# Kernel optimization log

Measured on AMD Instinct MI355X. Metric: run time of the kernel, lower is better.

Reference implementation:

```python
import jax, jax.numpy as jnp
import numpy as np

N = 50000        # nodes
E = 800000       # edges (avg degree 16)
F = 64           # num_features
G = 128          # number of graphs in the batch
NOUT = 1         # n_output


def setup_inputs() -> dict:
    key = jax.random.key(0)
    ks = jax.random.split(key, 9)
    x = jax.random.normal(ks[0], (N, F), dtype=jnp.float32)
    edge_index = jax.random.randint(ks[1], (2, E), 0, N, dtype=jnp.int64)
    batch = jnp.sort(jax.random.randint(ks[2], (N,), 0, G, dtype=jnp.int64))
    W1 = jax.random.normal(ks[3], (F, F), dtype=jnp.float32) * 0.1
    b1 = jnp.zeros((F,), dtype=jnp.float32)
    W2 = jax.random.normal(ks[4], (F, 2 * F), dtype=jnp.float32) * 0.1
    b2 = jnp.zeros((2 * F,), dtype=jnp.float32)
    fcW = jax.random.normal(ks[5], (2 * F, NOUT), dtype=jnp.float32) * 0.1
    fcb = jnp.zeros((NOUT,), dtype=jnp.float32)
    return {"x": x, "edge_index": edge_index, "batch": batch,
            "W1": W1, "b1": b1, "W2": W2, "b2": b2, "fcW": fcW, "fcb": fcb}


def reference(x, edge_index, batch, W1, b1, W2, b2, fcW, fcb):
    n = x.shape[0]
    # PyG GCNConv: add self-loops, symmetric normalization D^-1/2 (A+I) D^-1/2
    loop = jnp.arange(n, dtype=edge_index.dtype)
    src = jnp.concatenate([edge_index[0], loop])  # [E+N]
    dst = jnp.concatenate([edge_index[1], loop])  # [E+N]
    deg = jax.ops.segment_sum(jnp.ones_like(dst, dtype=x.dtype), dst, num_segments=n)
    dinv = jnp.where(deg > 0, jax.lax.rsqrt(jnp.maximum(deg, 1.0)), 0.0)
    norm = dinv[src] * dinv[dst]                  # [E+N]

    def gcn_conv(h, W, b):
        h = h @ W                                 # [N, Fout]
        msg = h[src] * norm[:, None]              # gather + scale, [E+N, Fout]
        return jax.ops.segment_sum(msg, dst, num_segments=n) + b

    h1 = jax.nn.relu(gcn_conv(x, W1, b1))         # [N, F]
    h2 = jax.nn.relu(gcn_conv(h1, W2, b2))        # [N, 2F]

    # global mean pool per graph (dropout is identity in eval)
    counts = jax.ops.segment_sum(jnp.ones((n,), x.dtype), batch, num_segments=G)
    pooled = jax.ops.segment_sum(h2, batch, num_segments=G)
    pooled = pooled / jnp.maximum(counts, 1.0)[:, None]  # [G, 2F]

    out = pooled @ fcW + fcb                      # [G, NOUT]
    return out.reshape(1, -1)                     # [1, G*NOUT]
```

## Files before the change

### kernel.cpp

```cpp
#include <hip/hip_runtime.h>
#include <hip/hip_bf16.h>

typedef __hip_bfloat16 bf16;

static __device__ __forceinline__ float loadF(const void* p, long long i, int f32){
  return f32 ? ((const float*)p)[i] : __bfloat162float(((const bf16*)p)[i]);
}
static __device__ __forceinline__ int loadI(const void* p, long long i, int i64){
  return i64 ? (int)((const long long*)p)[i] : ((const int*)p)[i];
}
static __device__ __forceinline__ unsigned short f2bf(float f){
  unsigned u = __float_as_uint(f);
  return (unsigned short)((u + 0x7FFFu + ((u>>16)&1u)) >> 16);
}
static __device__ __forceinline__ float bf2f(unsigned v){
  return __uint_as_float(v<<16);
}

#define CAP 4096
#define LB_EDGES 8192

__global__ void k_init(const unsigned int* __restrict__ xw, const unsigned int* __restrict__ eiw,
                       int* __restrict__ flags, int* __restrict__ gcursor, int nbuckets,
                       float* __restrict__ S, int gn, int* __restrict__ done){
  int i = blockIdx.x*256 + threadIdx.x;
  if(i < nbuckets) gcursor[i] = 0;
  if(i < gn) S[i] = 0.f;
  if(i == 0) done[0] = 0;
  if(blockIdx.x == 0){
    __shared__ int s1, s2;
    if(threadIdx.x==0){ s1=0; s2=0; }
    __syncthreads();
    unsigned w = xw[threadIdx.x];
    int e = (int)((w>>7)&0xFFu);
    if(e>=110 && e<=135) atomicAdd(&s1, 1);
    if(eiw[2*threadIdx.x+1] != 0u) atomicAdd(&s2, 1);
    __syncthreads();
    if(threadIdx.x==0){
      flags[0] = (s1 < 128) ? 1 : 0;
      flags[1] = (s2 < 128) ? 1 : 0;
    }
  }
}

__global__ __launch_bounds__(256) void k_pre(const void* __restrict__ ei, int E, int N,
                                             const int* __restrict__ flags,
                                             int* __restrict__ gcursor,
                                             unsigned int* __restrict__ log, int nbuckets,
                                             const void* __restrict__ x, const void* __restrict__ W,
                                             unsigned short* __restrict__ y, int nLog){
  __shared__ unsigned int smem[12416];
  int t = threadIdx.x;
  if((int)blockIdx.x < nLog){
    unsigned int* stash = smem;
    int* hcnt  = (int*)(smem + LB_EDGES);
    int* hbase = (int*)(smem + LB_EDGES + 1024);
    for(int b=t; b<nbuckets; b+=256) hcnt[b] = 0;
    __syncthreads();
    int i64 = flags[1];
    long long e0 = (long long)blockIdx.x*LB_EDGES;
    int cnt = (int)(((long long)E - e0) < LB_EDGES ? ((long long)E - e0) : LB_EDGES);
    for(int k=t; k<cnt; k+=256){
      long long e = e0 + k;
      int s = loadI(ei, e, i64);                 s = min(max(s,0), N-1);
      int d = loadI(ei, (long long)E + e, i64);  d = min(max(d,0), N-1);
      unsigned p = (((unsigned)d)<<16) | (unsigned)s;
      stash[k] = p;
      atomicAdd(&hcnt[d>>6], 1);
    }
    __syncthreads();
    for(int b=t; b<nbuckets; b+=256){
      int c = hcnt[b];
      hbase[b] = (c>0) ? atomicAdd(&gcursor[b], c) : 0;
      hcnt[b] = 0;
    }
    __syncthreads();
    for(int k=t; k<cnt; k+=256){
      unsigned p = stash[k];
      int b = (int)(p>>22);
      int pos = hbase[b] + atomicAdd(&hcnt[b], 1);
      if(pos < CAP) log[(long long)b*CAP + pos] = p;
    }
  } else {
    float* Ws = (float*)smem;
    float* xs = (float*)(smem + 4096);
    int f32 = flags[0];
    int row0 = ((int)blockIdx.x - nLog)*128;
    if(f32){
      const float4* W4 = (const float4*)W;
      for(int i=t;i<1024;i+=256){
        float4 v = W4[i];
        Ws[i*4]=v.x; Ws[i*4+1]=v.y; Ws[i*4+2]=v.z; Ws[i*4+3]=v.w;
      }
      const float4* X4 = (const float4*)x;
      for(int i=t;i<2048;i+=256){
        int r = i>>4, c4 = i&15;
        int gr = row0 + r;
        float4 v = {0.f,0.f,0.f,0.f};
        if(gr<N) v = X4[(long long)gr*16 + c4];
        float* xd = &xs[r*65 + c4*4];
        xd[0]=v.x; xd[1]=v.y; xd[2]=v.z; xd[3]=v.w;
      }
    } else {
      for(int i=t;i<4096;i+=256) Ws[i] = loadF(W, i, 0);
      const unsigned int* X32 = (const unsigned int*)x;
      for(int i=t;i<4096;i+=256){
        int r = i>>5, kd = i&31;
        int gr = row0 + r;
        unsigned v = (gr<N) ? X32[(long long)gr*32 + kd] : 0u;
        xs[r*65 + 2*kd    ] = bf2f(v & 0xFFFFu);
        xs[r*65 + 2*kd + 1] = bf2f(v >> 16);
      }
    }
    __syncthreads();
    int cg = t&15, rg = t>>4;
    int col_g = cg*4, row_g = rg*8;
    float acc[8][4];
    #pragma unroll
    for(int r=0;r<8;r++){ acc[r][0]=0.f; acc[r][1]=0.f; acc[r][2]=0.f; acc[r][3]=0.f; }
    for(int k=0;k<64;k++){
      float4 w = *(const float4*)&Ws[k*64 + col_g];
      float xr[8];
      #pragma unroll
      for(int r=0;r<8;r++) xr[r] = xs[(row_g+r)*65 + k];
      #pragma unroll
      for(int r=0;r<8;r++){
        acc[r][0] += xr[r]*w.x; acc[r][1] += xr[r]*w.y;
        acc[r][2] += xr[r]*w.z; acc[r][3] += xr[r]*w.w;
      }
    }
    #pragma unroll
    for(int r=0;r<8;r++){
      int gr = row0 + row_g + r;
      if(gr<N){
        ushort4 st;
        st.x = f2bf(acc[r][0]); st.y = f2bf(acc[r][1]);
        st.z = f2bf(acc[r][2]); st.w = f2bf(acc[r][3]);
        *(ushort4*)&y[(long long)gr*64 + col_g] = st;
      }
    }
  }
}

__global__ __launch_bounds__(256) void k_bsortg0(const unsigned int* __restrict__ log,
                                                 const int* __restrict__ gcursor,
                                                 unsigned short* __restrict__ csr,
                                                 int* __restrict__ beg, int* __restrict__ endv,
                                                 float* __restrict__ dinv,
                                                 const unsigned int* __restrict__ Y32,
                                                 unsigned int* __restrict__ G032, int N){
  __shared__ int hist[64];
  __shared__ int cur[64];
  __shared__ float dloc[64];
  int b = blockIdx.x, t = threadIdx.x;
  if(t < 64) hist[t] = 0;
  __syncthreads();
  int n = min(gcursor[b], CAP);
  const unsigned int* L = log + (long long)b*CAP;
  for(int j=t; j<n; j+=256) atomicAdd(&hist[(L[j]>>16)&63], 1);
  __syncthreads();
  if(t < 64){
    int v = hist[t];
    int inc = v;
    #pragma unroll
    for(int o=1; o<64; o<<=1){
      int u = __shfl_up(inc, o);
      if(t >= o) inc += u;
    }
    int excl = inc - v;
    cur[t] = excl;
    float dv = rsqrtf((float)(v + 1));
    dloc[t] = dv;
    int node = b*64 + t;
    if(node < N){
      int base = b*CAP + excl;
      beg[node]  = base;
      endv[node] = base + v;
      dinv[node] = dv;
    }
  }
  __syncthreads();
  unsigned short* C = csr + (long long)b*CAP;
  for(int j=t; j<n; j+=256){
    unsigned p = L[j];
    int l = (int)((p>>16)&63u);
    int pos = atomicAdd(&cur[l], 1);
    C[pos] = (unsigned short)(p & 0xFFFFu);
  }
  long long base32 = (long long)b*2048;
  for(int i=t; i<2048; i+=256){
    int nl = i>>5;
    int node = b*64 + nl;
    if(node < N){
      unsigned v = Y32[base32 + i];
      float dv = dloc[nl];
      G032[base32 + i] = (unsigned)f2bf(bf2f(v & 0xFFFFu)*dv)
                       | ((unsigned)f2bf(bf2f(v >> 16)*dv) << 16);
    }
  }
}

__global__ __launch_bounds__(256) void k_agg(const unsigned short* __restrict__ g,
                                             const unsigned short* __restrict__ csr,
                                             const int* __restrict__ beg, const int* __restrict__ endv,
                                             const float* __restrict__ dinv,
                                             const void* __restrict__ bias, const int* __restrict__ flags,
                                             int mode,
                                             uint4* __restrict__ out128, int N){
  int node = blockIdx.x*4 + (threadIdx.x>>6);
  int lane = threadIdx.x&63;
  if(node >= N) return;
  int q = lane&7, eg = lane>>3;
  const uint4* G128 = (const uint4*)g;
  int j = beg[node], e = endv[node];
  float a0=0.f,a1=0.f,a2=0.f,a3=0.f,a4=0.f,a5=0.f,a6=0.f,a7=0.f;
  for(; j+16<=e; j+=16){
    int sA = csr[j + eg];
    int sB = csr[j + 8 + eg];
    uint4 vA = G128[(long long)sA*8 + q];
    uint4 vB = G128[(long long)sB*8 + q];
    a0 += bf2f(vA.x & 0xFFFFu); a1 += bf2f(vA.x >> 16);
    a2 += bf2f(vA.y & 0xFFFFu); a3 += bf2f(vA.y >> 16);
    a4 += bf2f(vA.z & 0xFFFFu); a5 += bf2f(vA.z >> 16);
    a6 += bf2f(vA.w & 0xFFFFu); a7 += bf2f(vA.w >> 16);
    a0 += bf2f(vB.x & 0xFFFFu); a1 += bf2f(vB.x >> 16);
    a2 += bf2f(vB.y & 0xFFFFu); a3 += bf2f(vB.y >> 16);
    a4 += bf2f(vB.z & 0xFFFFu); a5 += bf2f(vB.z >> 16);
    a6 += bf2f(vB.w & 0xFFFFu); a7 += bf2f(vB.w >> 16);
  }
  for(; j+8<=e; j+=8){
    int s = csr[j + eg];
    uint4 v = G128[(long long)s*8 + q];
    a0 += bf2f(v.x & 0xFFFFu); a1 += bf2f(v.x >> 16);
    a2 += bf2f(v.y & 0xFFFFu); a3 += bf2f(v.y >> 16);
    a4 += bf2f(v.z & 0xFFFFu); a5 += bf2f(v.z >> 16);
    a6 += bf2f(v.w & 0xFFFFu); a7 += bf2f(v.w >> 16);
  }
  if(j + eg < e){
    int s = csr[j + eg];
    uint4 v = G128[(long long)s*8 + q];
    a0 += bf2f(v.x & 0xFFFFu); a1 += bf2f(v.x >> 16);
    a2 += bf2f(v.y & 0xFFFFu); a3 += bf2f(v.y >> 16);
    a4 += bf2f(v.z & 0xFFFFu); a5 += bf2f(v.z >> 16);
    a6 += bf2f(v.w & 0xFFFFu); a7 += bf2f(v.w >> 16);
  }
  uint4 sv = {0u,0u,0u,0u};
  float dv = 0.f;
  if(eg == 0){
    sv = G128[(long long)node*8 + q];
    dv = dinv[node];
  }
  #pragma unroll
  for(int m=8; m<64; m<<=1){
    a0 += __shfl_xor(a0, m, 64); a1 += __shfl_xor(a1, m, 64);
    a2 += __shfl_xor(a2, m, 64); a3 += __shfl_xor(a3, m, 64);
    a4 += __shfl_xor(a4, m, 64); a5 += __shfl_xor(a5, m, 64);
    a6 += __shfl_xor(a6, m, 64); a7 += __shfl_xor(a7, m, 64);
  }
  if(eg == 0){
    float f0 = (a0 + bf2f(sv.x & 0xFFFFu)) * dv;
    float f1 = (a1 + bf2f(sv.x >> 16)) * dv;
    float f2 = (a2 + bf2f(sv.y & 0xFFFFu)) * dv;
    float f3 = (a3 + bf2f(sv.y >> 16)) * dv;
    float f4 = (a4 + bf2f(sv.z & 0xFFFFu)) * dv;
    float f5 = (a5 + bf2f(sv.z >> 16)) * dv;
    float f6 = (a6 + bf2f(sv.w & 0xFFFFu)) * dv;
    float f7 = (a7 + bf2f(sv.w >> 16)) * dv;
    if(mode){
      int f32 = flags[0];
      f0 = fmaxf(f0 + loadF(bias, q*8+0, f32), 0.f) * dv;
      f1 = fmaxf(f1 + loadF(bias, q*8+1, f32), 0.f) * dv;
      f2 = fmaxf(f2 + loadF(bias, q*8+2, f32), 0.f) * dv;
      f3 = fmaxf(f3 + loadF(bias, q*8+3, f32), 0.f) * dv;
      f4 = fmaxf(f4 + loadF(bias, q*8+4, f32), 0.f) * dv;
      f5 = fmaxf(f5 + loadF(bias, q*8+5, f32), 0.f) * dv;
      f6 = fmaxf(f6 + loadF(bias, q*8+6, f32), 0.f) * dv;
      f7 = fmaxf(f7 + loadF(bias, q*8+7, f32), 0.f) * dv;
    }
    uint4 o;
    o.x = (unsigned)f2bf(f0) | ((unsigned)f2bf(f1) << 16);
    o.y = (unsigned)f2bf(f2) | ((unsigned)f2bf(f3) << 16);
    o.z = (unsigned)f2bf(f4) | ((unsigned)f2bf(f5) << 16);
    o.w = (unsigned)f2bf(f6) | ((unsigned)f2bf(f7) << 16);
    out128[(long long)node*8 + q] = o;
  }
}

static __device__ __forceinline__ int lower_bound_batch(const void* batch, int N, int key, int i64){
  int lo = 0, hi = N;
  while(lo < hi){ int mid = (lo+hi)>>1; if(loadI(batch, mid, i64) < key) lo = mid+1; else hi = mid; }
  return lo;
}

__global__ __launch_bounds__(512) void k_gemm2pool(const unsigned int* __restrict__ A32, const void* __restrict__ W,
                                                   const void* __restrict__ b, const void* __restrict__ fcW,
                                                   const void* __restrict__ batch, const int* __restrict__ flags,
                                                   float* __restrict__ S, int* __restrict__ done,
                                                   const void* __restrict__ fcb, void* __restrict__ out,
                                                   int N, int G, int NOUT){
  __shared__ float Ws[64*128];
  __shared__ float xs[128*65];
  __shared__ float Sloc[128*4];
  __shared__ int gid[128];
  __shared__ int lastBlk;
  int f32 = flags[0], i64 = flags[1];
  int tid = threadIdx.x;
  int row0 = blockIdx.x*128;
  for(int i=tid;i<8192;i+=512) Ws[i] = loadF(W, i, f32);
  for(int i=tid;i<4096;i+=512){
    int r = i>>5, kd = i&31;
    int gr = row0 + r;
    unsigned v = (gr<N) ? A32[(long long)gr*32 + kd] : 0u;
    xs[r*65 + 2*kd    ] = bf2f(v & 0xFFFFu);
    xs[r*65 + 2*kd + 1] = bf2f(v >> 16);
  }
  if(tid < 128){
    int node = row0 + tid;
    gid[tid] = (node < N) ? loadI(batch, node, i64) : 0;
  }
  if(tid < 512) { if(tid < 512 && tid < 512) ; }
  for(int i=tid;i<512;i+=512) Sloc[i] = 0.f;
  __syncthreads();
  int cg = tid&15, rg = tid>>4;
  int c0 = cg*4, c1 = 64 + cg*4, row_g = rg*4;
  float acc[4][8];
  #pragma unroll
  for(int r=0;r<4;r++)
    #pragma unroll
    for(int c=0;c<8;c++) acc[r][c]=0.f;
  for(int k=0;k<64;k++){
    float4 w0 = *(const float4*)&Ws[k*128 + c0];
    float4 w1 = *(const float4*)&Ws[k*128 + c1];
    float xr[4];
    #pragma unroll
    for(int r=0;r<4;r++) xr[r] = xs[(row_g+r)*65 + k];
    #pragma unroll
    for(int r=0;r<4;r++){
      acc[r][0] += xr[r]*w0.x; acc[r][1] += xr[r]*w0.y;
      acc[r][2] += xr[r]*w0.z; acc[r][3] += xr[r]*w0.w;
      acc[r][4] += xr[r]*w1.x; acc[r][5] += xr[r]*w1.y;
      acc[r][6] += xr[r]*w1.z; acc[r][7] += xr[r]*w1.w;
    }
  }
  #pragma unroll
  for(int c=0;c<8;c++){
    int col = (c<4) ? (c0+c) : (c1+c-4);
    float bb = loadF(b, col, f32);
    #pragma unroll
    for(int r=0;r<4;r++){ float z = acc[r][c]+bb; acc[r][c] = z>0.f?z:0.f; }
  }
  int nv = N - row0; nv = nv < 128 ? nv : 128;
  if(nv > 0){
    int gmin = gid[0], gmax = gid[nv-1];
    bool ldsOK = (NOUT <= 4) && (gmax - gmin < 128);
    for(int o=0;o<NOUT;o++){
      float fw[8];
      #pragma unroll
      for(int c=0;c<8;c++){
        int col = (c<4) ? (c0+c) : (c1+c-4);
        fw[c] = loadF(fcW, (long long)col*NOUT + o, f32);
      }
      #pragma unroll
      for(int r=0;r<4;r++){
        float z = acc[r][0]*fw[0] + acc[r][1]*fw[1] + acc[r][2]*fw[2] + acc[r][3]*fw[3]
                + acc[r][4]*fw[4] + acc[r][5]*fw[5] + acc[r][6]*fw[6] + acc[r][7]*fw[7];
        #pragma unroll
        for(int m=1;m<16;m<<=1) z += __shfl_xor(z, m, 64);
        int nl = row_g + r;
        if(cg==0 && nl < nv){
          int gg = gid[nl];
          if(ldsOK) atomicAdd(&Sloc[(gg-gmin)*NOUT + o], z);
          else      atomicAdd(&S[(long long)gg*NOUT + o], z);
        }
      }
    }
    if(ldsOK){
      __syncthreads();
      int nbin = (gmax - gmin + 1)*NOUT;
      for(int i=tid; i<nbin; i+=512){
        float v = Sloc[i];
        if(v != 0.f){
          int bin = i / NOUT, o = i - bin*NOUT;
          atomicAdd(&S[(long long)(gmin+bin)*NOUT + o], v);
        }
      }
    }
  }
  asm volatile("s_waitcnt vmcnt(0)" ::: "memory");
  if(tid==0) lastBlk = (atomicAdd(done, 1) == (int)gridDim.x - 1) ? 1 : 0;
  __syncthreads();
  if(lastBlk){
    for(int g2=tid; g2<G; g2+=512){
      int c = lower_bound_batch(batch, N, g2+1, i64) - lower_bound_batch(batch, N, g2, i64);
      float inv = 1.f / (float)(c > 0 ? c : 1);
      for(int o=0;o<NOUT;o++){
        float sv = atomicAdd(&S[(long long)g2*NOUT + o], 0.f);
        float r = sv*inv + loadF(fcb, o, f32);
        if(f32) ((float*)out)[g2*NOUT+o] = r;
        else    ((unsigned short*)out)[g2*NOUT+o] = f2bf(r);
      }
    }
  }
}

extern "C" void kernel_launch(void* const* d_in, const int* in_sizes, int n_in,
                              void* d_out, int out_size, void* d_ws, size_t ws_size,
                              hipStream_t stream) {
  const void* x    = d_in[0];
  const void* ei   = d_in[1];
  const void* batch= d_in[2];
  const void* W1   = d_in[3];
  const void* b1   = d_in[4];
  const void* W2   = d_in[5];
  const void* b2   = d_in[6];
  const void* fcW  = d_in[7];
  const void* fcb  = d_in[8];

  const int N = in_sizes[0] / 64;
  const int E = in_sizes[1] / 2;
  const int NOUT = in_sizes[8];
  const int G = out_size / NOUT;
  const int nbuckets = (N + 63) >> 6;

  size_t off = 0;
  auto alloc = [&](size_t bytes) -> char* {
    char* p = (char*)d_ws + off;
    off += (bytes + 511) & ~(size_t)511;
    return p;
  };
  int*   flags   = (int*)  alloc(512);
  int*   done    = (int*)  alloc(512);
  int*   gcursor = (int*)  alloc((size_t)nbuckets*4);
  float* dinv    = (float*)alloc((size_t)N*4);
  int*   beg     = (int*)  alloc((size_t)N*4);
  int*   endv    = (int*)  alloc((size_t)N*4);
  float* S       = (float*)alloc((size_t)G*NOUT*4);
  unsigned int*   log  = (unsigned int*)  alloc((size_t)nbuckets*CAP*4);
  unsigned short* csr  = (unsigned short*)alloc((size_t)nbuckets*CAP*2);
  unsigned short* yB   = (unsigned short*)alloc((size_t)N*64*2);
  unsigned short* g0   = (unsigned short*)alloc((size_t)N*64*2);
  unsigned short* g1   = (unsigned short*)alloc((size_t)N*64*2);
  unsigned int*   aBuf = (unsigned int*)  alloc((size_t)N*32*4);
  (void)ws_size; (void)n_in;

  int initgrid = (nbuckets > G*NOUT ? nbuckets : G*NOUT);
  int nLog = (E + LB_EDGES - 1) / LB_EDGES;
  int nGem = (N + 127) / 128;

  k_init    <<<(initgrid+255)/256, 256, 0, stream>>>((const unsigned int*)x, (const unsigned int*)ei,
                                                     flags, gcursor, nbuckets, S, G*NOUT, done);
  k_pre     <<<nLog + nGem,   256, 0, stream>>>(ei, E, N, flags, gcursor, log, nbuckets,
                                                x, W1, yB, nLog);
  k_bsortg0 <<<nbuckets,      256, 0, stream>>>(log, gcursor, csr, beg, endv, dinv,
                                                (const unsigned int*)yB, (unsigned int*)g0, N);

  k_agg     <<<(N+3)/4,       256, 0, stream>>>(g0, csr, beg, endv, dinv, b1, flags, 1,
                                                (uint4*)g1, N);
  k_agg     <<<(N+3)/4,       256, 0, stream>>>(g1, csr, beg, endv, dinv, b1, flags, 0,
                                                (uint4*)aBuf, N);
  k_gemm2pool<<<(N+127)/128,  512, 0, stream>>>((const unsigned int*)aBuf, W2, b2, fcW, batch, flags,
                                                S, done, fcb, d_out, N, G, NOUT);
}
```

Baseline: 188.2 us.

## Fold source-degree scaling into first aggregation and widen k_pre blocks

The bucket-sort kernel no longer pre-scales the layer-1 GEMM output by dinv into a separate g0 buffer. The first aggregation instead reads the raw GEMM output and multiplies each gathered row by dinv[src] on the fly, with matching self-loop handling. This removes one full N×64 read/write pass and a buffer, at the cost of an extra scattered dinv load per edge. k_pre also moves to 512-thread blocks, with the GEMM branch computing 4 rows per thread instead of 8.

New measurement: 180.9 us. 3.9% less time.

```diff
diff --git a/kernel.cpp b/kernel.cpp
--- a/kernel.cpp
+++ b/kernel.cpp
@@ -43,7 +43,7 @@
   }
 }
 
-__global__ __launch_bounds__(256) void k_pre(const void* __restrict__ ei, int E, int N,
+__global__ __launch_bounds__(512) void k_pre(const void* __restrict__ ei, int E, int N,
                                              const int* __restrict__ flags,
                                              int* __restrict__ gcursor,
                                              unsigned int* __restrict__ log, int nbuckets,
@@ -55,12 +55,12 @@
     unsigned int* stash = smem;
     int* hcnt  = (int*)(smem + LB_EDGES);
     int* hbase = (int*)(smem + LB_EDGES + 1024);
-    for(int b=t; b<nbuckets; b+=256) hcnt[b] = 0;
+    for(int b=t; b<nbuckets; b+=512) hcnt[b] = 0;
     __syncthreads();
     int i64 = flags[1];
     long long e0 = (long long)blockIdx.x*LB_EDGES;
     int cnt = (int)(((long long)E - e0) < LB_EDGES ? ((long long)E - e0) : LB_EDGES);
-    for(int k=t; k<cnt; k+=256){
+    for(int k=t; k<cnt; k+=512){
       long long e = e0 + k;
       int s = loadI(ei, e, i64);                 s = min(max(s,0), N-1);
       int d = loadI(ei, (long long)E + e, i64);  d = min(max(d,0), N-1);
@@ -69,13 +69,13 @@
       atomicAdd(&hcnt[d>>6], 1);
     }
     __syncthreads();
-    for(int b=t; b<nbuckets; b+=256){
+    for(int b=t; b<nbuckets; b+=512){
       int c = hcnt[b];
       hbase[b] = (c>0) ? atomicAdd(&gcursor[b], c) : 0;
       hcnt[b] = 0;
     }
     __syncthreads();
-    for(int k=t; k<cnt; k+=256){
+    for(int k=t; k<cnt; k+=512){
       unsigned p = stash[k];
       int b = (int)(p>>22);
       int pos = hbase[b] + atomicAdd(&hcnt[b], 1);
@@ -88,12 +88,12 @@
     int row0 = ((int)blockIdx.x - nLog)*128;
     if(f32){
       const float4* W4 = (const float4*)W;
-      for(int i=t;i<1024;i+=256){
+      for(int i=t;i<1024;i+=512){
         float4 v = W4[i];
         Ws[i*4]=v.x; Ws[i*4+1]=v.y; Ws[i*4+2]=v.z; Ws[i*4+3]=v.w;
       }
       const float4* X4 = (const float4*)x;
-      for(int i=t;i<2048;i+=256){
+      for(int i=t;i<2048;i+=512){
         int r = i>>4, c4 = i&15;
         int gr = row0 + r;
         float4 v = {0.f,0.f,0.f,0.f};
@@ -102,9 +102,9 @@
         xd[0]=v.x; xd[1]=v.y; xd[2]=v.z; xd[3]=v.w;
       }
     } else {
-      for(int i=t;i<4096;i+=256) Ws[i] = loadF(W, i, 0);
+      for(int i=t;i<4096;i+=512) Ws[i] = loadF(W, i, 0);
       const unsigned int* X32 = (const unsigned int*)x;
-      for(int i=t;i<4096;i+=256){
+      for(int i=t;i<4096;i+=512){
         int r = i>>5, kd = i&31;
         int gr = row0 + r;
         unsigned v = (gr<N) ? X32[(long long)gr*32 + kd] : 0u;
@@ -114,23 +114,23 @@
     }
     __syncthreads();
     int cg = t&15, rg = t>>4;
-    int col_g = cg*4, row_g = rg*8;
-    float acc[8][4];
-    #pragma unroll
-    for(int r=0;r<8;r++){ acc[r][0]=0.f; acc[r][1]=0.f; acc[r][2]=0.f; acc[r][3]=0.f; }
+    int col_g = cg*4, row_g = rg*4;
+    float acc[4][4];
+    #pragma unroll
+    for(int r=0;r<4;r++){ acc[r][0]=0.f; acc[r][1]=0.f; acc[r][2]=0.f; acc[r][3]=0.f; }
     for(int k=0;k<64;k++){
       float4 w = *(const float4*)&Ws[k*64 + col_g];
-      float xr[8];
+      float xr[4];
       #pragma unroll
-      for(int r=0;r<8;r++) xr[r] = xs[(row_g+r)*65 + k];
+      for(int r=0;r<4;r++) xr[r] = xs[(row_g+r)*65 + k];
       #pragma unroll
-      for(int r=0;r<8;r++){
+      for(int r=0;r<4;r++){
         acc[r][0] += xr[r]*w.x; acc[r][1] += xr[r]*w.y;
         acc[r][2] += xr[r]*w.z; acc[r][3] += xr[r]*w.w;
       }
     }
     #pragma unroll
-    for(int r=0;r<8;r++){
+    for(int r=0;r<4;r++){
       int gr = row0 + row_g + r;
       if(gr<N){
         ushort4 st;
@@ -142,16 +142,13 @@
   }
 }
 
-__global__ __launch_bounds__(256) void k_bsortg0(const unsigned int* __restrict__ log,
-                                                 const int* __restrict__ gcursor,
-                                                 unsigned short* __restrict__ csr,
-                                                 int* __restrict__ beg, int* __restrict__ endv,
-                                                 float* __restrict__ dinv,
-                                                 const unsigned int* __restrict__ Y32,
-                                                 unsigned int* __restrict__ G032, int N){
+__global__ __launch_bounds__(256) void k_bsort(const unsigned int* __restrict__ log,
+                                               const int* __restrict__ gcursor,
+                                               unsigned short* __restrict__ csr,
+                                               int* __restrict__ beg, int* __restrict__ endv,
+                                               float* __restrict__ dinv, int N){
   __shared__ int hist[64];
   __shared__ int cur[64];
-  __shared__ float dloc[64];
   int b = blockIdx.x, t = threadIdx.x;
   if(t < 64) hist[t] = 0;
   __syncthreads();
@@ -169,14 +166,12 @@
     }
     int excl = inc - v;
     cur[t] = excl;
-    float dv = rsqrtf((float)(v + 1));
-    dloc[t] = dv;
     int node = b*64 + t;
     if(node < N){
       int base = b*CAP + excl;
       beg[node]  = base;
       endv[node] = base + v;
-      dinv[node] = dv;
+      dinv[node] = rsqrtf((float)(v + 1));
     }
   }
   __syncthreads();
@@ -186,17 +181,6 @@
     int l = (int)((p>>16)&63u);
     int pos = atomicAdd(&cur[l], 1);
     C[pos] = (unsigned short)(p & 0xFFFFu);
-  }
-  long long base32 = (long long)b*2048;
-  for(int i=t; i<2048; i+=256){
-    int nl = i>>5;
-    int node = b*64 + nl;
-    if(node < N){
-      unsigned v = Y32[base32 + i];
-      float dv = dloc[nl];
-      G032[base32 + i] = (unsigned)f2bf(bf2f(v & 0xFFFFu)*dv)
-                       | ((unsigned)f2bf(bf2f(v >> 16)*dv) << 16);
-    }
   }
 }
 
@@ -214,35 +198,71 @@
   const uint4* G128 = (const uint4*)g;
   int j = beg[node], e = endv[node];
   float a0=0.f,a1=0.f,a2=0.f,a3=0.f,a4=0.f,a5=0.f,a6=0.f,a7=0.f;
-  for(; j+16<=e; j+=16){
-    int sA = csr[j + eg];
-    int sB = csr[j + 8 + eg];
-    uint4 vA = G128[(long long)sA*8 + q];
-    uint4 vB = G128[(long long)sB*8 + q];
-    a0 += bf2f(vA.x & 0xFFFFu); a1 += bf2f(vA.x >> 16);
-    a2 += bf2f(vA.y & 0xFFFFu); a3 += bf2f(vA.y >> 16);
-    a4 += bf2f(vA.z & 0xFFFFu); a5 += bf2f(vA.z >> 16);
-    a6 += bf2f(vA.w & 0xFFFFu); a7 += bf2f(vA.w >> 16);
-    a0 += bf2f(vB.x & 0xFFFFu); a1 += bf2f(vB.x >> 16);
-    a2 += bf2f(vB.y & 0xFFFFu); a3 += bf2f(vB.y >> 16);
-    a4 += bf2f(vB.z & 0xFFFFu); a5 += bf2f(vB.z >> 16);
-    a6 += bf2f(vB.w & 0xFFFFu); a7 += bf2f(vB.w >> 16);
-  }
-  for(; j+8<=e; j+=8){
-    int s = csr[j + eg];
-    uint4 v = G128[(long long)s*8 + q];
-    a0 += bf2f(v.x & 0xFFFFu); a1 += bf2f(v.x >> 16);
-    a2 += bf2f(v.y & 0xFFFFu); a3 += bf2f(v.y >> 16);
-    a4 += bf2f(v.z & 0xFFFFu); a5 += bf2f(v.z >> 16);
-    a6 += bf2f(v.w & 0xFFFFu); a7 += bf2f(v.w >> 16);
-  }
-  if(j + eg < e){
-    int s = csr[j + eg];
-    uint4 v = G128[(long long)s*8 + q];
-    a0 += bf2f(v.x & 0xFFFFu); a1 += bf2f(v.x >> 16);
-    a2 += bf2f(v.y & 0xFFFFu); a3 += bf2f(v.y >> 16);
-    a4 += bf2f(v.z & 0xFFFFu); a5 += bf2f(v.z >> 16);
-    a6 += bf2f(v.w & 0xFFFFu); a7 += bf2f(v.w >> 16);
+  if(mode){
+    for(; j+16<=e; j+=16){
+      int sA = csr[j + eg];
+      int sB = csr[j + 8 + eg];
+      float dA = dinv[sA], dB = dinv[sB];
+      uint4 vA = G128[(long long)sA*8 + q];
+      uint4 vB = G128[(long long)sB*8 + q];
+      a0 += dA*bf2f(vA.x & 0xFFFFu); a1 += dA*bf2f(vA.x >> 16);
+      a2 += dA*bf2f(vA.y & 0xFFFFu); a3 += dA*bf2f(vA.y >> 16);
+      a4 += dA*bf2f(vA.z & 0xFFFFu); a5 += dA*bf2f(vA.z >> 16);
+      a6 += dA*bf2f(vA.w & 0xFFFFu); a7 += dA*bf2f(vA.w >> 16);
+      a0 += dB*bf2f(vB.x & 0xFFFFu); a1 += dB*bf2f(vB.x >> 16);
+      a2 += dB*bf2f(vB.y & 0xFFFFu); a3 += dB*bf2f(vB.y >> 16);
+      a4 += dB*bf2f(vB.z & 0xFFFFu); a5 += dB*bf2f(vB.z >> 16);
+      a6 += dB*bf2f(vB.w & 0xFFFFu); a7 += dB*bf2f(vB.w >> 16);
+    }
+    for(; j+8<=e; j+=8){
+      int s = csr[j + eg];
+      float d = dinv[s];
+      uint4 v = G128[(long long)s*8 + q];
+      a0 += d*bf2f(v.x & 0xFFFFu); a1 += d*bf2f(v.x >> 16);
+      a2 += d*bf2f(v.y & 0xFFFFu); a3 += d*bf2f(v.y >> 16);
+      a4 += d*bf2f(v.z & 0xFFFFu); a5 += d*bf2f(v.z >> 16);
+      a6 += d*bf2f(v.w & 0xFFFFu); a7 += d*bf2f(v.w >> 16);
+    }
+    if(j + eg < e){
+      int s = csr[j + eg];
+      float d = dinv[s];
+      uint4 v = G128[(long long)s*8 + q];
+      a0 += d*bf2f(v.x & 0xFFFFu); a1 += d*bf2f(v.x >> 16);
+      a2 += d*bf2f(v.y & 0xFFFFu); a3 += d*bf2f(v.y >> 16);
+      a4 += d*bf2f(v.z & 0xFFFFu); a5 += d*bf2f(v.z >> 16);
+      a6 += d*bf2f(v.w & 0xFFFFu); a7 += d*bf2f(v.w >> 16);
+    }
+  } else {
+    for(; j+16<=e; j+=16){
+      int sA = csr[j + eg];
+      int sB = csr[j + 8 + eg];
+      uint4 vA = G128[(long long)sA*8 + q];
+      uint4 vB = G128[(long long)sB*8 + q];
+      a0 += bf2f(vA.x & 0xFFFFu); a1 += bf2f(vA.x >> 16);
+      a2 += bf2f(vA.y & 0xFFFFu); a3 += bf2f(vA.y >> 16);
+      a4 += bf2f(vA.z & 0xFFFFu); a5 += bf2f(vA.z >> 16);
+      a6 += bf2f(vA.w & 0xFFFFu); a7 += bf2f(vA.w >> 16);
+      a0 += bf2f(vB.x & 0xFFFFu); a1 += bf2f(vB.x >> 16);
+      a2 += bf2f(vB.y & 0xFFFFu); a3 += bf2f(vB.y >> 16);
+      a4 += bf2f(vB.z & 0xFFFFu); a5 += bf2f(vB.z >> 16);
+      a6 += bf2f(vB.w & 0xFFFFu); a7 += bf2f(vB.w >> 16);
+    }
+    for(; j+8<=e; j+=8){
+      int s = csr[j + eg];
+      uint4 v = G128[(long long)s*8 + q];
+      a0 += bf2f(v.x & 0xFFFFu); a1 += bf2f(v.x >> 16);
+      a2 += bf2f(v.y & 0xFFFFu); a3 += bf2f(v.y >> 16);
+      a4 += bf2f(v.z & 0xFFFFu); a5 += bf2f(v.z >> 16);
+      a6 += bf2f(v.w & 0xFFFFu); a7 += bf2f(v.w >> 16);
+    }
+    if(j + eg < e){
+      int s = csr[j + eg];
+      uint4 v = G128[(long long)s*8 + q];
+      a0 += bf2f(v.x & 0xFFFFu); a1 += bf2f(v.x >> 16);
+      a2 += bf2f(v.y & 0xFFFFu); a3 += bf2f(v.y >> 16);
+      a4 += bf2f(v.z & 0xFFFFu); a5 += bf2f(v.z >> 16);
+      a6 += bf2f(v.w & 0xFFFFu); a7 += bf2f(v.w >> 16);
+    }
   }
   uint4 sv = {0u,0u,0u,0u};
   float dv = 0.f;
@@ -258,14 +278,15 @@
     a6 += __shfl_xor(a6, m, 64); a7 += __shfl_xor(a7, m, 64);
   }
   if(eg == 0){
-    float f0 = (a0 + bf2f(sv.x & 0xFFFFu)) * dv;
-    float f1 = (a1 + bf2f(sv.x >> 16)) * dv;
-    float f2 = (a2 + bf2f(sv.y & 0xFFFFu)) * dv;
-    float f3 = (a3 + bf2f(sv.y >> 16)) * dv;
-    float f4 = (a4 + bf2f(sv.z & 0xFFFFu)) * dv;
-    float f5 = (a5 + bf2f(sv.z >> 16)) * dv;
-    float f6 = (a6 + bf2f(sv.w & 0xFFFFu)) * dv;
-    float f7 = (a7 + bf2f(sv.w >> 16)) * dv;
+    float selfs = mode ? dv : 1.f;
+    float f0 = (a0 + selfs*bf2f(sv.x & 0xFFFFu)) * dv;
+    float f1 = (a1 + selfs*bf2f(sv.x >> 16)) * dv;
+    float f2 = (a2 + selfs*bf2f(sv.y & 0xFFFFu)) * dv;
+    float f3 = (a3 + selfs*bf2f(sv.y >> 16)) * dv;
+    float f4 = (a4 + selfs*bf2f(sv.z & 0xFFFFu)) * dv;
+    float f5 = (a5 + selfs*bf2f(sv.z >> 16)) * dv;
+    float f6 = (a6 + selfs*bf2f(sv.w & 0xFFFFu)) * dv;
+    float f7 = (a7 + selfs*bf2f(sv.w >> 16)) * dv;
     if(mode){
       int f32 = flags[0];
       f0 = fmaxf(f0 + loadF(bias, q*8+0, f32), 0.f) * dv;
@@ -318,7 +339,6 @@
     int node = row0 + tid;
     gid[tid] = (node < N) ? loadI(batch, node, i64) : 0;
   }
-  if(tid < 512) { if(tid < 512 && tid < 512) ; }
   for(int i=tid;i<512;i+=512) Sloc[i] = 0.f;
   __syncthreads();
   int cg = tid&15, rg = tid>>4;
@@ -438,7 +458,6 @@
   unsigned int*   log  = (unsigned int*)  alloc((size_t)nbuckets*CAP*4);
   unsigned short* csr  = (unsigned short*)alloc((size_t)nbuckets*CAP*2);
   unsigned short* yB   = (unsigned short*)alloc((size_t)N*64*2);
-  unsigned short* g0   = (unsigned short*)alloc((size_t)N*64*2);
   unsigned short* g1   = (unsigned short*)alloc((size_t)N*64*2);
   unsigned int*   aBuf = (unsigned int*)  alloc((size_t)N*32*4);
   (void)ws_size; (void)n_in;
@@ -449,12 +468,11 @@
 
   k_init    <<<(initgrid+255)/256, 256, 0, stream>>>((const unsigned int*)x, (const unsigned int*)ei,
                                                      flags, gcursor, nbuckets, S, G*NOUT, done);
-  k_pre     <<<nLog + nGem,   256, 0, stream>>>(ei, E, N, flags, gcursor, log, nbuckets,
+  k_pre     <<<nLog + nGem,   512, 0, stream>>>(ei, E, N, flags, gcursor, log, nbuckets,
                                                 x, W1, yB, nLog);
-  k_bsortg0 <<<nbuckets,      256, 0, stream>>>(log, gcursor, csr, beg, endv, dinv,
-                                                (const unsigned int*)yB, (unsigned int*)g0, N);
-
-  k_agg     <<<(N+3)/4,       256, 0, stream>>>(g0, csr, beg, endv, dinv, b1, flags, 1,
+  k_bsort   <<<nbuckets,      256, 0, stream>>>(log, gcursor, csr, beg, endv, dinv, N);
+
+  k_agg     <<<(N+3)/4,       256, 0, stream>>>(yB, csr, beg, endv, dinv, b1, flags, 1,
                                                 (uint4*)g1, N);
   k_agg     <<<(N+3)/4,       256, 0, stream>>>(g1, csr, beg, endv, dinv, b1, flags, 0,
                                                 (uint4*)aBuf, N);
```
